# Kernel tuning notes

Measured on AMD Instinct MI355X. Metric: run time of the kernel, lower is better.

Reference implementation:

```python
import jax, jax.numpy as jnp
import numpy as np

N_NODES = 20000
LN_EPS = 1e-5


def setup_inputs() -> dict:
    key = jax.random.key(0)
    ks = jax.random.split(key, 8)
    N, E, D_IN, D_H = N_NODES, 320000, 128, 256
    x = jax.random.normal(ks[0], (N, D_IN), dtype=jnp.float32)
    edge_index = jax.random.randint(ks[1], (2, E), 0, N, dtype=jnp.int64)
    edge_weight = jax.random.uniform(ks[2], (E,), dtype=jnp.float32)
    # Glorot-ish scaled weights
    W1 = jax.random.normal(ks[3], (D_IN, D_H), dtype=jnp.float32) / np.sqrt(D_IN)
    W2 = jax.random.normal(ks[4], (D_H, D_H), dtype=jnp.float32) / np.sqrt(D_H)
    Wres = jax.random.normal(ks[5], (D_IN, D_H), dtype=jnp.float32) / np.sqrt(D_IN)
    return {
        "x": x, "edge_index": edge_index, "edge_weight": edge_weight,
        "W1": W1, "b1": jnp.zeros((D_H,), jnp.float32),
        "W2": W2, "b2": jnp.zeros((D_H,), jnp.float32),
        "Wres": Wres, "bres": jnp.zeros((D_H,), jnp.float32),
        "gamma1": jnp.ones((D_H,), jnp.float32), "beta1": jnp.zeros((D_H,), jnp.float32),
        "gamma2": jnp.ones((D_H,), jnp.float32), "beta2": jnp.zeros((D_H,), jnp.float32),
    }


def _gcn_conv(x, W, b, src, dst, w, n):
    # PyG GCNConv: linear transform, then sym-normalized scatter-add aggregation
    h = x @ W  # [N, D_H]
    deg = jax.ops.segment_sum(w, dst, num_segments=n)  # in-degree incl. self loops
    dinv = jnp.where(deg > 0, jax.lax.rsqrt(deg), 0.0)
    norm = dinv[src] * w * dinv[dst]  # [E+N]
    out = jax.ops.segment_sum(norm[:, None] * h[src], dst, num_segments=n)
    return out + b


def _layer_norm(x, gamma, beta):
    mu = jnp.mean(x, axis=-1, keepdims=True)
    var = jnp.mean(jnp.square(x - mu), axis=-1, keepdims=True)
    return (x - mu) * jax.lax.rsqrt(var + LN_EPS) * gamma + beta


def reference(x, edge_index, edge_weight, W1, b1, W2, b2, Wres, bres,
              gamma1, beta1, gamma2, beta2):
    n = x.shape[0]
    loop = jnp.arange(n, dtype=edge_index.dtype)
    # add self loops with weight 1 (add_self_loops=True)
    src = jnp.concatenate([edge_index[0], loop])
    dst = jnp.concatenate([edge_index[1], loop])
    w = jnp.concatenate([edge_weight, jnp.ones((n,), edge_weight.dtype)])

    # hop 0: conv -> relu (dropout p=0, eval) -> residual proj -> LayerNorm
    delta = jax.nn.relu(_gcn_conv(x, W1, b1, src, dst, w, n))
    h = _layer_norm(x @ Wres + bres + delta, gamma1, beta1)

    # hop 1 (last): conv -> residual -> LayerNorm (no relu)
    delta = _gcn_conv(h, W2, b2, src, dst, w, n)
    h = _layer_norm(h + delta, gamma2, beta2)
    return h
```

## Files before the change

kernel.cpp:

```cpp
#include <hip/hip_runtime.h>
#include <stdint.h>


constexpr int DIN = 128;
constexpr int DH  = 256;
#define LN_EPS 1e-5f

typedef __attribute__((ext_vector_type(8))) short bf16x8;
typedef __attribute__((ext_vector_type(4))) short bf16x4;
typedef __attribute__((ext_vector_type(4))) float f32x4;

__device__ __forceinline__ short f2bf(float f) {
  union { float f; unsigned u; } v; v.f = f;
  unsigned r = v.u + 0x7fffu + ((v.u >> 16) & 1u);
  return (short)(r >> 16);
}
__device__ __forceinline__ float bf2f(short b) {
  union { unsigned u; float f; } v; v.u = ((unsigned)(unsigned short)b) << 16;
  return v.f;
}

__device__ __forceinline__ int probe_m64(const unsigned* ei, int E) {
  int lane = threadIdx.x & 63;
  long long stride = (E >= 64) ? (E / 64) : 1;
  long long li = (long long)lane * stride;
  if (li >= E) li = 0;
  unsigned v = ei[2 * li + 1];
  return __ballot(v != 0u) == 0ull;
}

__device__ __forceinline__ int eidx(const void* ei, long long e, int m64) {
  return m64 ? (int)((const long long*)ei)[e] : ((const int*)ei)[e];
}


__global__ __launch_bounds__(256) void k_prep(const float* __restrict__ x,
                                              short* __restrict__ xb,
                                              const float* __restrict__ W1,
                                              const float* __restrict__ Wres,
                                              const float* __restrict__ W2,
                                              short* __restrict__ W1t,
                                              short* __restrict__ Wrt,
                                              short* __restrict__ W2t,
                                              const void* ei,
                                              const float* __restrict__ ew,
                                              float* deg, int* cnt,
                                              int N, int E) {
  const int NXV = N * DIN / 8;
  const int NW  = DIN * DH;
  const int NW2 = DH * DH;
  int idx = blockIdx.x * 256 + threadIdx.x;
  if (idx < NXV) {
    f32x4 a = ((const f32x4*)x)[idx * 2];
    f32x4 b = ((const f32x4*)x)[idx * 2 + 1];
    bf16x8 o;
    o[0] = f2bf(a[0]); o[1] = f2bf(a[1]); o[2] = f2bf(a[2]); o[3] = f2bf(a[3]);
    o[4] = f2bf(b[0]); o[5] = f2bf(b[1]); o[6] = f2bf(b[2]); o[7] = f2bf(b[3]);
    ((bf16x8*)xb)[idx] = o;
    return;
  }
  idx -= NXV;
  if (idx < NW) {
    int n = idx / DIN, k = idx % DIN;
    W1t[idx] = f2bf(W1[k * DH + n]);
    return;
  }
  idx -= NW;
  if (idx < NW) {
    int n = idx / DIN, k = idx % DIN;
    Wrt[idx] = f2bf(Wres[k * DH + n]);
    return;
  }
  idx -= NW;
  if (idx < NW2) {
    int n = idx / DH, k = idx % DH;
    W2t[idx] = f2bf(W2[k * DH + n]);
    return;
  }
  idx -= NW2;
  int m64 = probe_m64((const unsigned*)ei, E);
  if (idx < E) {
    int d = eidx(ei, (long long)E + idx, m64);
    atomicAdd(&deg[d], ew[idx]);
    atomicAdd(&cnt[d], 1);
  }
}


__global__ __launch_bounds__(1024) void k_scan(const int* __restrict__ cnt,
                                               float* deg, int* rowptr,
                                               int* cursor, int n) {
  for (int i = threadIdx.x; i < n; i += 1024) deg[i] = rsqrtf(1.0f + deg[i]);

  constexpr int MAXI = 32;
  int items = (n + 1023) / 1024;
  int tid = threadIdx.x, lane = tid & 63, wv = tid >> 6;
  int base = tid * items;
  int v[MAXI];
  int tot = 0;
#pragma unroll 4
  for (int j = 0; j < items; ++j) {
    int i = base + j;
    v[j] = (i < n) ? cnt[i] : 0;
    tot += v[j];
  }
  int sc = tot;
#pragma unroll
  for (int off = 1; off < 64; off <<= 1) {
    int t = __shfl_up(sc, off, 64);
    if (lane >= off) sc += t;
  }
  __shared__ int wsum[16];
  if (lane == 63) wsum[wv] = sc;
  __syncthreads();
  if (wv == 0 && lane < 16) {
    int s = wsum[lane];
#pragma unroll
    for (int off = 1; off < 16; off <<= 1) {
      int t = __shfl_up(s, off, 64);
      if (lane >= off) s += t;
    }
    wsum[lane] = s;
  }
  __syncthreads();
  int prefix = (sc - tot) + ((wv > 0) ? wsum[wv - 1] : 0);
  if (tid == 0) { rowptr[0] = 0; cursor[0] = 0; }
  int run = prefix;
#pragma unroll 4
  for (int j = 0; j < items; ++j) {
    int i = base + j;
    run += v[j];
    if (i < n) { rowptr[i + 1] = run; cursor[i + 1] = run; }
  }
}


__global__ __launch_bounds__(256) void k_fill(const void* ei,
                                              const float* __restrict__ w,
                                              const float* __restrict__ dinv,
                                              int* cursor, int* srcs,
                                              float* norms, int E) {
  int m64 = probe_m64((const unsigned*)ei, E);
  int e = blockIdx.x * 256 + threadIdx.x;
  if (e >= E) return;
  int s = eidx(ei, e, m64);
  int d = eidx(ei, (long long)E + e, m64);
  int p = atomicAdd(&cursor[d], 1);
  srcs[p] = s;
  norms[p] = dinv[s] * w[e] * dinv[d];
}


__global__ __launch_bounds__(256) void k_agg128(const short* __restrict__ T,
                                                const int* __restrict__ rowptr,
                                                const int* __restrict__ srcs,
                                                const float* __restrict__ norms,
                                                const float* __restrict__ dinv,
                                                short* __restrict__ out, int n) {
  int wv = threadIdx.x >> 6, lane = threadIdx.x & 63;
  int i = blockIdx.x * 4 + wv;
  if (i >= n) return;
  int h = lane >> 5;
  int c = (lane & 31) * 4;
  float a0 = 0.f, a1 = 0.f, a2 = 0.f, a3 = 0.f;
  int e = rowptr[i] + h, end = rowptr[i + 1];
  for (; e + 6 < end; e += 8) {
    int s0 = srcs[e], s1 = srcs[e + 2], s2 = srcs[e + 4], s3 = srcs[e + 6];
    float w0 = norms[e], w1 = norms[e + 2], w2 = norms[e + 4], w3 = norms[e + 6];
    bf16x4 v0 = *(const bf16x4*)(T + (long long)s0 * DIN + c);
    bf16x4 v1 = *(const bf16x4*)(T + (long long)s1 * DIN + c);
    bf16x4 v2 = *(const bf16x4*)(T + (long long)s2 * DIN + c);
    bf16x4 v3 = *(const bf16x4*)(T + (long long)s3 * DIN + c);
    a0 += w0 * bf2f(v0[0]) + w1 * bf2f(v1[0]) + w2 * bf2f(v2[0]) + w3 * bf2f(v3[0]);
    a1 += w0 * bf2f(v0[1]) + w1 * bf2f(v1[1]) + w2 * bf2f(v2[1]) + w3 * bf2f(v3[1]);
    a2 += w0 * bf2f(v0[2]) + w1 * bf2f(v1[2]) + w2 * bf2f(v2[2]) + w3 * bf2f(v3[2]);
    a3 += w0 * bf2f(v0[3]) + w1 * bf2f(v1[3]) + w2 * bf2f(v2[3]) + w3 * bf2f(v3[3]);
  }
  for (; e < end; e += 2) {
    int s = srcs[e];
    float w = norms[e];
    bf16x4 v = *(const bf16x4*)(T + (long long)s * DIN + c);
    a0 += w * bf2f(v[0]); a1 += w * bf2f(v[1]);
    a2 += w * bf2f(v[2]); a3 += w * bf2f(v[3]);
  }
  a0 += __shfl_xor(a0, 32, 64); a1 += __shfl_xor(a1, 32, 64);
  a2 += __shfl_xor(a2, 32, 64); a3 += __shfl_xor(a3, 32, 64);
  if (h == 0) {
    float sw = dinv[i] * dinv[i];
    bf16x4 sv = *(const bf16x4*)(T + (long long)i * DIN + c);
    bf16x4 o;
    o[0] = f2bf(a0 + sw * bf2f(sv[0]));
    o[1] = f2bf(a1 + sw * bf2f(sv[1]));
    o[2] = f2bf(a2 + sw * bf2f(sv[2]));
    o[3] = f2bf(a3 + sw * bf2f(sv[3]));
    *(bf16x4*)(out + (long long)i * DIN + c) = o;
  }
}

__global__ __launch_bounds__(256) void k_agg256(const short* __restrict__ T,
                                                const int* __restrict__ rowptr,
                                                const int* __restrict__ srcs,
                                                const float* __restrict__ norms,
                                                const float* __restrict__ dinv,
                                                short* __restrict__ out, int n) {
  int wv = threadIdx.x >> 6, lane = threadIdx.x & 63;
  int i = blockIdx.x * 4 + wv;
  if (i >= n) return;
  int h = lane >> 5;
  int c = (lane & 31) * 8;
  float acc[8];
#pragma unroll
  for (int k = 0; k < 8; ++k) acc[k] = 0.f;
  int e = rowptr[i] + h, end = rowptr[i + 1];
  for (; e + 6 < end; e += 8) {
    int s0 = srcs[e], s1 = srcs[e + 2], s2 = srcs[e + 4], s3 = srcs[e + 6];
    float w0 = norms[e], w1 = norms[e + 2], w2 = norms[e + 4], w3 = norms[e + 6];
    bf16x8 v0 = *(const bf16x8*)(T + (long long)s0 * DH + c);
    bf16x8 v1 = *(const bf16x8*)(T + (long long)s1 * DH + c);
    bf16x8 v2 = *(const bf16x8*)(T + (long long)s2 * DH + c);
    bf16x8 v3 = *(const bf16x8*)(T + (long long)s3 * DH + c);
#pragma unroll
    for (int k = 0; k < 8; ++k)
      acc[k] += w0 * bf2f(v0[k]) + w1 * bf2f(v1[k]) +
                w2 * bf2f(v2[k]) + w3 * bf2f(v3[k]);
  }
  for (; e < end; e += 2) {
    int s = srcs[e];
    float w = norms[e];
    bf16x8 v = *(const bf16x8*)(T + (long long)s * DH + c);
#pragma unroll
    for (int k = 0; k < 8; ++k) acc[k] += w * bf2f(v[k]);
  }
#pragma unroll
  for (int k = 0; k < 8; ++k) acc[k] += __shfl_xor(acc[k], 32, 64);
  if (h == 0) {
    float sw = dinv[i] * dinv[i];
    bf16x8 sv = *(const bf16x8*)(T + (long long)i * DH + c);
    bf16x8 o;
#pragma unroll
    for (int k = 0; k < 8; ++k) o[k] = f2bf(acc[k] + sw * bf2f(sv[k]));
    *(bf16x8*)(out + (long long)i * DH + c) = o;
  }
}


__global__ __launch_bounds__(64) void k_gemm_ln1(
    const short* __restrict__ Sx, const short* __restrict__ xb,
    const short* __restrict__ W1t, const short* __restrict__ Wrt,
    const float* __restrict__ b1, const float* __restrict__ bres,
    const float* __restrict__ g1, const float* __restrict__ be1,
    short* __restrict__ h1b, int M) {
  int lane = threadIdx.x & 63;
  int lr = lane & 15, lg = lane >> 4;
  int bm = blockIdx.x * 16;
  int ar = min(bm + lr, M - 1);

  f32x4 acc[16] = {};
#pragma unroll
  for (int ks = 0; ks < 4; ++ks) {
    bf16x8 a = *(const bf16x8*)(Sx + (long long)ar * DIN + ks * 32 + lg * 8);
#pragma unroll
    for (int ni = 0; ni < 16; ++ni) {
      bf16x8 b = *(const bf16x8*)(W1t + (ni * 16 + lr) * DIN + ks * 32 + lg * 8);
      acc[ni] = __builtin_amdgcn_mfma_f32_16x16x32_bf16(a, b, acc[ni], 0, 0, 0);
    }
  }
#pragma unroll
  for (int ni = 0; ni < 16; ++ni) {
    int col = ni * 16 + lr;
    float bb = b1[col], br = bres[col];
#pragma unroll
    for (int j = 0; j < 4; ++j)
      acc[ni][j] = fmaxf(acc[ni][j] + bb, 0.f) + br;
  }
#pragma unroll
  for (int ks = 0; ks < 4; ++ks) {
    bf16x8 a = *(const bf16x8*)(xb + (long long)ar * DIN + ks * 32 + lg * 8);
#pragma unroll
    for (int ni = 0; ni < 16; ++ni) {
      bf16x8 b = *(const bf16x8*)(Wrt + (ni * 16 + lr) * DIN + ks * 32 + lg * 8);
      acc[ni] = __builtin_amdgcn_mfma_f32_16x16x32_bf16(a, b, acc[ni], 0, 0, 0);
    }
  }
#pragma unroll
  for (int j = 0; j < 4; ++j) {
    int r = bm + lg * 4 + j;
    float s1 = 0.f, s2 = 0.f;
#pragma unroll
    for (int ni = 0; ni < 16; ++ni) {
      float v = acc[ni][j];
      s1 += v; s2 += v * v;
    }
#pragma unroll
    for (int m = 1; m < 16; m <<= 1) {
      s1 += __shfl_xor(s1, m, 64);
      s2 += __shfl_xor(s2, m, 64);
    }
    float mu = s1 * (1.f / 256.f);
    float rs = rsqrtf(s2 * (1.f / 256.f) - mu * mu + LN_EPS);
    if (r < M) {
#pragma unroll
      for (int ni = 0; ni < 16; ++ni) {
        int col = ni * 16 + lr;
        float y = (acc[ni][j] - mu) * rs * g1[col] + be1[col];
        h1b[(long long)r * DH + col] = f2bf(y);
      }
    }
  }
}


__global__ __launch_bounds__(64) void k_gemm_ln2(
    const short* __restrict__ Sh1, const short* __restrict__ h1b,
    const short* __restrict__ W2t, const float* __restrict__ b2,
    const float* __restrict__ g2, const float* __restrict__ be2,
    float* __restrict__ out, int M) {
  int lane = threadIdx.x & 63;
  int lr = lane & 15, lg = lane >> 4;
  int bm = blockIdx.x * 16;
  int ar = min(bm + lr, M - 1);

  f32x4 acc[16] = {};
#pragma unroll
  for (int ks = 0; ks < 8; ++ks) {
    bf16x8 a = *(const bf16x8*)(Sh1 + (long long)ar * DH + ks * 32 + lg * 8);
#pragma unroll
    for (int ni = 0; ni < 16; ++ni) {
      bf16x8 b = *(const bf16x8*)(W2t + (ni * 16 + lr) * DH + ks * 32 + lg * 8);
      acc[ni] = __builtin_amdgcn_mfma_f32_16x16x32_bf16(a, b, acc[ni], 0, 0, 0);
    }
  }
#pragma unroll
  for (int j = 0; j < 4; ++j) {
    int rr = min(bm + lg * 4 + j, M - 1);
#pragma unroll
    for (int ni = 0; ni < 16; ++ni) {
      int col = ni * 16 + lr;
      acc[ni][j] += b2[col] + bf2f(h1b[(long long)rr * DH + col]);
    }
  }
#pragma unroll
  for (int j = 0; j < 4; ++j) {
    int r = bm + lg * 4 + j;
    float s1 = 0.f, s2 = 0.f;
#pragma unroll
    for (int ni = 0; ni < 16; ++ni) {
      float v = acc[ni][j];
      s1 += v; s2 += v * v;
    }
#pragma unroll
    for (int m = 1; m < 16; m <<= 1) {
      s1 += __shfl_xor(s1, m, 64);
      s2 += __shfl_xor(s2, m, 64);
    }
    float mu = s1 * (1.f / 256.f);
    float rs = rsqrtf(s2 * (1.f / 256.f) - mu * mu + LN_EPS);
    if (r < M) {
#pragma unroll
      for (int ni = 0; ni < 16; ++ni) {
        int col = ni * 16 + lr;
        out[(long long)r * DH + col] = (acc[ni][j] - mu) * rs * g2[col] + be2[col];
      }
    }
  }
}


extern "C" void kernel_launch(void* const* d_in, const int* in_sizes, int n_in,
                              void* d_out, int out_size, void* d_ws,
                              size_t ws_size, hipStream_t stream) {
  const float* x    = (const float*)d_in[0];
  const void*  ei   = d_in[1];
  const float* ew   = (const float*)d_in[2];
  const float* W1   = (const float*)d_in[3];
  const float* b1   = (const float*)d_in[4];
  const float* W2   = (const float*)d_in[5];
  const float* b2   = (const float*)d_in[6];
  const float* Wres = (const float*)d_in[7];
  const float* bres = (const float*)d_in[8];
  const float* g1   = (const float*)d_in[9];
  const float* be1  = (const float*)d_in[10];
  const float* g2   = (const float*)d_in[11];
  const float* be2  = (const float*)d_in[12];

  const int N = in_sizes[0] / DIN;
  const int E = in_sizes[2];

  char* ws = (char*)d_ws;
  auto alloc = [&](size_t bytes) -> char* {
    char* p = ws;
    ws += (bytes + 255) & ~(size_t)255;
    return p;
  };
  short* xb     = (short*)alloc((size_t)N * DIN * 2);
  short* W1t    = (short*)alloc((size_t)DIN * DH * 2);
  short* Wrt    = (short*)alloc((size_t)DIN * DH * 2);
  short* W2t    = (short*)alloc((size_t)DH * DH * 2);
  short* Sx     = (short*)alloc((size_t)N * DIN * 2);
  short* h1b    = (short*)alloc((size_t)N * DH * 2);
  short* Sh1    = (short*)alloc((size_t)N * DH * 2);
  int*   cnt    = (int*)alloc((size_t)N * 8);
  float* deg    = (float*)(cnt + N);
  int*   rowptr = (int*)alloc((size_t)(N + 1) * 4);
  int*   cursor = (int*)alloc((size_t)(N + 1) * 4);
  int*   srcs   = (int*)alloc((size_t)E * 4);
  float* norms  = (float*)alloc((size_t)E * 4);

  hipMemsetAsync(cnt, 0, (size_t)N * 8, stream);

  int prep_items = N * DIN / 8 + 2 * DIN * DH + DH * DH + E;
  k_prep<<<(prep_items + 255) / 256, 256, 0, stream>>>(
      x, xb, W1, Wres, W2, W1t, Wrt, W2t, ei, ew, deg, cnt, N, E);
  k_scan<<<1, 1024, 0, stream>>>(cnt, deg, rowptr, cursor, N);
  k_fill<<<(E + 255) / 256, 256, 0, stream>>>(ei, ew, deg, cursor, srcs, norms, E);

  k_agg128<<<(N + 3) / 4, 256, 0, stream>>>(xb, rowptr, srcs, norms, deg, Sx, N);
  k_gemm_ln1<<<(N + 15) / 16, 64, 0, stream>>>(Sx, xb, W1t, Wrt, b1, bres, g1,
                                               be1, h1b, N);
  k_agg256<<<(N + 3) / 4, 256, 0, stream>>>(h1b, rowptr, srcs, norms, deg, Sh1, N);
  k_gemm_ln2<<<(N + 15) / 16, 64, 0, stream>>>(Sh1, h1b, W2t, b2, g2, be2,
                                               (float*)d_out, N);
}
```

Measured before the change: 262.5 us.

## Split GEMM+LayerNorm column tiles across four waves with shared-memory staging

Both GEMM+LayerNorm kernels now use 256-thread blocks where each of four waves computes 64 of the 256 output columns for a 16-row tile, instead of one wave computing all 256. The A rows (and the residual rows in layer 2) are staged once into LDS, and the LayerNorm row statistics are combined across waves through a small shared buffer and a barrier. This cuts per-wave register pressure (4 accumulators instead of 16) and increases parallelism per tile. The cost is extra barriers and LDS traffic, and each wave still reads its weight slice directly from global memory.

New measurement: 261.7 us. No clear change (-0.3%).

```diff
diff --git a/kernel.cpp b/kernel.cpp
--- a/kernel.cpp
+++ b/kernel.cpp
@@ -244,30 +244,42 @@
 }
 
 
-__global__ __launch_bounds__(64) void k_gemm_ln1(
+__global__ __launch_bounds__(256) void k_gemm_ln1(
     const short* __restrict__ Sx, const short* __restrict__ xb,
     const short* __restrict__ W1t, const short* __restrict__ Wrt,
     const float* __restrict__ b1, const float* __restrict__ bres,
     const float* __restrict__ g1, const float* __restrict__ be1,
     short* __restrict__ h1b, int M) {
-  int lane = threadIdx.x & 63;
+  __shared__ short As[16][DIN + 8];
+  __shared__ short Xs[16][DIN + 8];
+  __shared__ float red1[4][16], red2[4][16];
+  int tid = threadIdx.x;
+  int wv = tid >> 6, lane = tid & 63;
   int lr = lane & 15, lg = lane >> 4;
   int bm = blockIdx.x * 16;
-  int ar = min(bm + lr, M - 1);
-
-  f32x4 acc[16] = {};
+
+  {
+    int row = tid >> 4, ch = tid & 15;
+    int gr = min(bm + row, M - 1);
+    *(bf16x8*)(&As[row][ch * 8]) = *(const bf16x8*)(Sx + (long long)gr * DIN + ch * 8);
+    *(bf16x8*)(&Xs[row][ch * 8]) = *(const bf16x8*)(xb + (long long)gr * DIN + ch * 8);
+  }
+  __syncthreads();
+
+  f32x4 acc[4] = {};
 #pragma unroll
   for (int ks = 0; ks < 4; ++ks) {
-    bf16x8 a = *(const bf16x8*)(Sx + (long long)ar * DIN + ks * 32 + lg * 8);
-#pragma unroll
-    for (int ni = 0; ni < 16; ++ni) {
-      bf16x8 b = *(const bf16x8*)(W1t + (ni * 16 + lr) * DIN + ks * 32 + lg * 8);
+    bf16x8 a = *(const bf16x8*)(&As[lr][ks * 32 + lg * 8]);
+#pragma unroll
+    for (int ni = 0; ni < 4; ++ni) {
+      int col = (wv * 4 + ni) * 16 + lr;
+      bf16x8 b = *(const bf16x8*)(W1t + col * DIN + ks * 32 + lg * 8);
       acc[ni] = __builtin_amdgcn_mfma_f32_16x16x32_bf16(a, b, acc[ni], 0, 0, 0);
     }
   }
 #pragma unroll
-  for (int ni = 0; ni < 16; ++ni) {
-    int col = ni * 16 + lr;
+  for (int ni = 0; ni < 4; ++ni) {
+    int col = (wv * 4 + ni) * 16 + lr;
     float bb = b1[col], br = bres[col];
 #pragma unroll
     for (int j = 0; j < 4; ++j)
@@ -275,33 +287,39 @@
   }
 #pragma unroll
   for (int ks = 0; ks < 4; ++ks) {
-    bf16x8 a = *(const bf16x8*)(xb + (long long)ar * DIN + ks * 32 + lg * 8);
-#pragma unroll
-    for (int ni = 0; ni < 16; ++ni) {
-      bf16x8 b = *(const bf16x8*)(Wrt + (ni * 16 + lr) * DIN + ks * 32 + lg * 8);
+    bf16x8 a = *(const bf16x8*)(&Xs[lr][ks * 32 + lg * 8]);
+#pragma unroll
+    for (int ni = 0; ni < 4; ++ni) {
+      int col = (wv * 4 + ni) * 16 + lr;
+      bf16x8 b = *(const bf16x8*)(Wrt + col * DIN + ks * 32 + lg * 8);
       acc[ni] = __builtin_amdgcn_mfma_f32_16x16x32_bf16(a, b, acc[ni], 0, 0, 0);
     }
   }
 #pragma unroll
   for (int j = 0; j < 4; ++j) {
-    int r = bm + lg * 4 + j;
-    float s1 = 0.f, s2 = 0.f;
-#pragma unroll
-    for (int ni = 0; ni < 16; ++ni) {
-      float v = acc[ni][j];
-      s1 += v; s2 += v * v;
-    }
+    float s1 = acc[0][j] + acc[1][j] + acc[2][j] + acc[3][j];
+    float s2 = acc[0][j] * acc[0][j] + acc[1][j] * acc[1][j] +
+               acc[2][j] * acc[2][j] + acc[3][j] * acc[3][j];
 #pragma unroll
     for (int m = 1; m < 16; m <<= 1) {
       s1 += __shfl_xor(s1, m, 64);
       s2 += __shfl_xor(s2, m, 64);
     }
+    if (lr == 0) { red1[wv][lg * 4 + j] = s1; red2[wv][lg * 4 + j] = s2; }
+  }
+  __syncthreads();
+#pragma unroll
+  for (int j = 0; j < 4; ++j) {
+    int row = lg * 4 + j;
+    float s1 = red1[0][row] + red1[1][row] + red1[2][row] + red1[3][row];
+    float s2 = red2[0][row] + red2[1][row] + red2[2][row] + red2[3][row];
     float mu = s1 * (1.f / 256.f);
     float rs = rsqrtf(s2 * (1.f / 256.f) - mu * mu + LN_EPS);
+    int r = bm + row;
     if (r < M) {
 #pragma unroll
-      for (int ni = 0; ni < 16; ++ni) {
-        int col = ni * 16 + lr;
+      for (int ni = 0; ni < 4; ++ni) {
+        int col = (wv * 4 + ni) * 16 + lr;
         float y = (acc[ni][j] - mu) * rs * g1[col] + be1[col];
         h1b[(long long)r * DH + col] = f2bf(y);
       }
@@ -310,55 +328,76 @@
 }
 
 
-__global__ __launch_bounds__(64) void k_gemm_ln2(
+__global__ __launch_bounds__(256) void k_gemm_ln2(
     const short* __restrict__ Sh1, const short* __restrict__ h1b,
     const short* __restrict__ W2t, const float* __restrict__ b2,
     const float* __restrict__ g2, const float* __restrict__ be2,
     float* __restrict__ out, int M) {
-  int lane = threadIdx.x & 63;
+  __shared__ short As[16][DH + 8];
+  __shared__ short Hs[16][DH + 8];
+  __shared__ float red1[4][16], red2[4][16];
+  int tid = threadIdx.x;
+  int wv = tid >> 6, lane = tid & 63;
   int lr = lane & 15, lg = lane >> 4;
   int bm = blockIdx.x * 16;
-  int ar = min(bm + lr, M - 1);
-
-  f32x4 acc[16] = {};
+
+  {
+#pragma unroll
+    for (int q = 0; q < 2; ++q) {
+      int cidx = q * 256 + tid;
+      int row = cidx >> 5, ch = cidx & 31;
+      int gr = min(bm + row, M - 1);
+      *(bf16x8*)(&As[row][ch * 8]) = *(const bf16x8*)(Sh1 + (long long)gr * DH + ch * 8);
+      *(bf16x8*)(&Hs[row][ch * 8]) = *(const bf16x8*)(h1b + (long long)gr * DH + ch * 8);
+    }
+  }
+  __syncthreads();
+
+  f32x4 acc[4] = {};
 #pragma unroll
   for (int ks = 0; ks < 8; ++ks) {
-    bf16x8 a = *(const bf16x8*)(Sh1 + (long long)ar * DH + ks * 32 + lg * 8);
-#pragma unroll
-    for (int ni = 0; ni < 16; ++ni) {
-      bf16x8 b = *(const bf16x8*)(W2t + (ni * 16 + lr) * DH + ks * 32 + lg * 8);
+    bf16x8 a = *(const bf16x8*)(&As[lr][ks * 32 + lg * 8]);
+#pragma unroll
+    for (int ni = 0; ni < 4; ++ni) {
+      int col = (wv * 4 + ni) * 16 + lr;
+      bf16x8 b = *(const bf16x8*)(W2t + col * DH + ks * 32 + lg * 8);
       acc[ni] = __builtin_amdgcn_mfma_f32_16x16x32_bf16(a, b, acc[ni], 0, 0, 0);
     }
   }
 #pragma unroll
   for (int j = 0; j < 4; ++j) {
-    int rr = min(bm + lg * 4 + j, M - 1);
-#pragma unroll
-    for (int ni = 0; ni < 16; ++ni) {
-      int col = ni * 16 + lr;
-      acc[ni][j] += b2[col] + bf2f(h1b[(long long)rr * DH + col]);
+    int row = lg * 4 + j;
+#pragma unroll
+    for (int ni = 0; ni < 4; ++ni) {
+      int col = (wv * 4 + ni) * 16 + lr;
+      acc[ni][j] += b2[col] + bf2f(Hs[row][col]);
     }
   }
 #pragma unroll
   for (int j = 0; j < 4; ++j) {
-    int r = bm + lg * 4 + j;
-    float s1 = 0.f, s2 = 0.f;
-#pragma unroll
-    for (int ni = 0; ni < 16; ++ni) {
-      float v = acc[ni][j];
-      s1 += v; s2 += v * v;
-    }
+    float s1 = acc[0][j] + acc[1][j] + acc[2][j] + acc[3][j];
+    float s2 = acc[0][j] * acc[0][j] + acc[1][j] * acc[1][j] +
+               acc[2][j] * acc[2][j] + acc[3][j] * acc[3][j];
 #pragma unroll
     for (int m = 1; m < 16; m <<= 1) {
       s1 += __shfl_xor(s1, m, 64);
       s2 += __shfl_xor(s2, m, 64);
     }
+    if (lr == 0) { red1[wv][lg * 4 + j] = s1; red2[wv][lg * 4 + j] = s2; }
+  }
+  __syncthreads();
+#pragma unroll
+  for (int j = 0; j < 4; ++j) {
+    int row = lg * 4 + j;
+    float s1 = red1[0][row] + red1[1][row] + red1[2][row] + red1[3][row];
+    float s2 = red2[0][row] + red2[1][row] + red2[2][row] + red2[3][row];
     float mu = s1 * (1.f / 256.f);
     float rs = rsqrtf(s2 * (1.f / 256.f) - mu * mu + LN_EPS);
+    int r = bm + row;
     if (r < M) {
 #pragma unroll
-      for (int ni = 0; ni < 16; ++ni) {
-        int col = ni * 16 + lr;
+      for (int ni = 0; ni < 4; ++ni) {
+        int col = (wv * 4 + ni) * 16 + lr;
         out[(long long)r * DH + col] = (acc[ni][j] - mu) * rs * g2[col] + be2[col];
       }
     }
@@ -415,9 +454,10 @@
   k_fill<<<(E + 255) / 256, 256, 0, stream>>>(ei, ew, deg, cursor, srcs, norms, E);
 
   k_agg128<<<(N + 3) / 4, 256, 0, stream>>>(xb, rowptr, srcs, norms, deg, Sx, N);
-  k_gemm_ln1<<<(N + 15) / 16, 64, 0, stream>>>(Sx, xb, W1t, Wrt, b1, bres, g1,
-                                               be1, h1b, N);
+  const int NB = (N + 15) / 16;
+  k_gemm_ln1<<<NB, 256, 0, stream>>>(Sx, xb, W1t, Wrt, b1, bres, g1, be1,
+                                     h1b, N);
   k_agg256<<<(N + 3) / 4, 256, 0, stream>>>(h1b, rowptr, srcs, norms, deg, Sh1, N);
-  k_gemm_ln2<<<(N + 15) / 16, 64, 0, stream>>>(Sh1, h1b, W2t, b2, g2, be2,
-                                               (float*)d_out, N);
-}
+  k_gemm_ln2<<<NB, 256, 0, stream>>>(Sh1, h1b, W2t, b2, g2, be2,
+                                     (float*)d_out, N);
+}
```
